# Performance work log

Hardware: AMD Instinct MI355X
Metric: run time of the kernel (lower is better)

Reference implementation:

```python
import jax, jax.numpy as jnp
import numpy as np

B, D, H, DH, NQ, NK = 64, 768, 8, 128, 256, 256


def _ln(x, g, b, eps=1e-5):
    m = x.mean(-1, keepdims=True)
    v = ((x - m) ** 2).mean(-1, keepdims=True)
    return (x - m) / jnp.sqrt(v + eps) * g + b


def setup_inputs() -> dict:
    key = jax.random.key(0)
    ks = jax.random.split(key, 16)
    w = lambda k, s: jax.random.normal(k, s, jnp.float32) * 0.02
    return {
        'emb_cause': jax.random.normal(ks[0], (B, D), jnp.float32),
        'emb_action': jax.random.normal(ks[1], (B, D), jnp.float32),
        'tok_cause': jax.random.normal(ks[2], (B, NK, D), jnp.float32),
        'tok_effect': jax.random.normal(ks[3], (B, NQ, D), jnp.float32),
        'fuse_ln_g': jnp.ones(2 * D), 'fuse_ln_b': jnp.zeros(2 * D),
        'fuse_w1': w(ks[4], (2 * D, D)), 'fuse_b1': jnp.zeros(D),
        'fuse_w2': w(ks[5], (D, D)), 'fuse_b2': jnp.zeros(D),
        'delta_ln_g': jnp.ones(D), 'delta_ln_b': jnp.zeros(D),
        'delta_w': w(ks[6], (D, D)), 'delta_b': jnp.zeros(D),
        'qg_w': w(ks[7], (D, H * DH)), 'qg_b': jnp.zeros(H * DH),
        'kg_w': w(ks[8], (D, H * DH)), 'kg_b': jnp.zeros(H * DH),
        'eff_ln_g': jnp.ones(D), 'eff_ln_b': jnp.zeros(D),
        'eff_w1': w(ks[9], (D, D)), 'eff_b1': jnp.zeros(D),
        'eff_w2': w(ks[10], (D, D)), 'eff_b2': jnp.zeros(D),
        'u_w': w(ks[11], (D, H * DH)),
        'v_w': w(ks[12], (D, H * DH)),
        'logit_scale': jnp.zeros(()),
    }


def reference(emb_cause, emb_action, tok_cause, tok_effect,
              fuse_ln_g, fuse_ln_b, fuse_w1, fuse_b1, fuse_w2, fuse_b2,
              delta_ln_g, delta_ln_b, delta_w, delta_b,
              qg_w, qg_b, kg_w, kg_b,
              eff_ln_g, eff_ln_b, eff_w1, eff_b1, eff_w2, eff_b2,
              u_w, v_w, logit_scale):
    # fuse: LN -> Linear -> GELU(exact) -> Linear (dropout = identity, eval)
    ctx_in = jnp.concatenate([emb_cause, emb_action], axis=-1)  # (B, 2D)
    h = jax.nn.gelu(_ln(ctx_in, fuse_ln_g, fuse_ln_b) @ fuse_w1 + fuse_b1, approximate=False)
    ctx = h @ fuse_w2 + fuse_b2  # (B, D)

    delta_e = _ln(ctx, delta_ln_g, delta_ln_b) @ delta_w + delta_b  # (B, D)
    pooled_effect = tok_effect.mean(axis=1)  # (B, D)
    e_shifted = pooled_effect + delta_e

    eh = jax.nn.gelu(_ln(ctx, eff_ln_g, eff_ln_b) @ eff_w1 + eff_b1, approximate=False)
    effect_pred = eh @ eff_w2 + eff_b2  # (B, D)

    q_gate = 1.0 + jnp.tanh(jax.nn.silu(ctx @ qg_w + qg_b)).reshape(B, H, DH)
    k_gate = 1.0 + jnp.tanh(jax.nn.silu(ctx @ kg_w + kg_b)).reshape(B, H, DH)

    # logit bias: torch code materializes (B,H,Nq,Nk,Dh); equivalent math is a
    # per-head inner product u.v (independent of q) broadcast over Nq.
    u = (e_shifted @ u_w).reshape(B, H, DH)            # (B, H, Dh)
    v = (tok_cause @ v_w).reshape(B, NK, H, DH)        # (B, Nk, H, Dh)
    bias = jnp.einsum('bhd,bkhd->bhk', u, v) / np.float32(np.sqrt(DH))
    logit_bias = jnp.exp(logit_scale) * jnp.broadcast_to(bias[:, :, None, :], (B, H, NQ, NK))

    return (q_gate, k_gate, e_shifted, delta_e, logit_bias, effect_pred)
```

## Files before the change

kernel.cpp:

```cpp
#include <hip/hip_runtime.h>
#include <math.h>

#define TPB 256

typedef float vf4 __attribute__((ext_vector_type(4)));

__global__ __launch_bounds__(256) void k_front(const float* __restrict__ ec, const float* __restrict__ ea,
                        const float* __restrict__ g, const float* __restrict__ bb,
                        float* __restrict__ o,
                        const float* __restrict__ tok_effect, float* __restrict__ pp)
{
    int t = threadIdx.x;
    if (blockIdx.x < 64) {
        int r = blockIdx.x;
        __shared__ float red[4];
        float v[6];
        float sum = 0.f;
#pragma unroll
        for (int j = 0; j < 6; ++j) {
            int c = t + j * TPB;
            float x = (c < 768) ? ec[r * 768 + c] : ea[r * 768 + (c - 768)];
            v[j] = x; sum += x;
        }
#pragma unroll
        for (int o_ = 32; o_ > 0; o_ >>= 1) sum += __shfl_xor(sum, o_);
        if ((t & 63) == 0) red[t >> 6] = sum;
        __syncthreads();
        sum = red[0] + red[1] + red[2] + red[3];
        float mean = sum * (1.0f / 1536.0f);
        __syncthreads();
        float s2 = 0.f;
#pragma unroll
        for (int j = 0; j < 6; ++j) { float d = v[j] - mean; s2 += d * d; }
#pragma unroll
        for (int o_ = 32; o_ > 0; o_ >>= 1) s2 += __shfl_xor(s2, o_);
        if ((t & 63) == 0) red[t >> 6] = s2;
        __syncthreads();
        s2 = red[0] + red[1] + red[2] + red[3];
        float rstd = rsqrtf(s2 * (1.0f / 1536.0f) + 1e-5f);
#pragma unroll
        for (int j = 0; j < 6; ++j) {
            int c = t + j * TPB;
            o[r * 1536 + c] = (v[j] - mean) * rstd * g[c] + bb[c];
        }
    } else {
        int m = blockIdx.x - 64;
        int cchunk = m % 3;
        int b = (m / 3) % 64;
        int qz = m / 192;
        int c = cchunk * TPB + t;
        const float* base = tok_effect + (size_t)(b * 256 + qz * 64) * 768 + c;
        float s = 0.f;
#pragma unroll 8
        for (int q = 0; q < 64; ++q) s += base[(size_t)q * 768];
        pp[(qz * 64 + b) * 768 + c] = s;
    }
}

struct GArgs {
    const float* X[4]; const float* W[4];
    int tile0[5];
    int nseg; int K; int kslice; int totN;
    float* part;
};

__global__ __launch_bounds__(256) void k_gemmp(GArgs A)
{
    const int ct = blockIdx.x, s = blockIdx.y;
    const int t = threadIdx.x;
    int seg = 0;
    while (seg + 1 < A.nseg && ct >= A.tile0[seg + 1]) ++seg;
    const float* __restrict__ X = A.X[seg];
    const float* __restrict__ W = A.W[seg];
    const int N = (A.tile0[seg + 1] - A.tile0[seg]) * 64;
    const int cb = (ct - A.tile0[seg]) * 64;
    const int tr4 = (t >> 4) << 2;
    const int tc4 = (t & 15) << 2;
    const int k0 = s * A.kslice;
    __shared__ float xs[32][64];
    __shared__ float wt[32][68];
    float acc[4][4] = {{0.f,0.f,0.f,0.f},{0.f,0.f,0.f,0.f},{0.f,0.f,0.f,0.f},{0.f,0.f,0.f,0.f}};
    for (int kc = 0; kc < A.kslice; kc += 32) {
        for (int n = t; n < 64 * 32; n += TPB) {
            int r = n >> 5, k = n & 31;
            xs[k][r] = X[r * A.K + k0 + kc + k];
        }
        for (int n = t; n < 32 * 64; n += TPB) {
            int k = n >> 6, c = n & 63;
            wt[k][c] = W[(size_t)(k0 + kc + k) * N + cb + c];
        }
        __syncthreads();
#pragma unroll
        for (int k = 0; k < 32; ++k) {
            float4 xv = *(const float4*)&xs[k][tr4];
            float4 wv = *(const float4*)&wt[k][tc4];
            acc[0][0] += xv.x * wv.x; acc[0][1] += xv.x * wv.y; acc[0][2] += xv.x * wv.z; acc[0][3] += xv.x * wv.w;
            acc[1][0] += xv.y * wv.x; acc[1][1] += xv.y * wv.y; acc[1][2] += xv.y * wv.z; acc[1][3] += xv.y * wv.w;
            acc[2][0] += xv.z * wv.x; acc[2][1] += xv.z * wv.y; acc[2][2] += xv.z * wv.z; acc[2][3] += xv.z * wv.w;
            acc[3][0] += xv.w * wv.x; acc[3][1] += xv.w * wv.y; acc[3][2] += xv.w * wv.z; acc[3][3] += xv.w * wv.w;
        }
        __syncthreads();
    }
    float* pp = A.part + (size_t)(s * 64 + tr4) * A.totN + ct * 64 + tc4;
#pragma unroll
    for (int i = 0; i < 4; ++i)
#pragma unroll
        for (int j = 0; j < 4; ++j)
            pp[i * A.totN + j] = acc[i][j];
}

struct EpiArgs {
    const float* part; const float* pp;
    const float* bias[4]; float* Y[4]; float* Y2[4];
    int col0[5]; int act[4]; int nseg; int totN; int S;
};

__global__ __launch_bounds__(256) void k_epi(EpiArgs A)
{
    int idx = blockIdx.x * TPB + threadIdx.x;
    if (idx >= 64 * A.totN) return;
    int r = idx / A.totN;
    int c = idx - r * A.totN;
    float v = 0.f;
    for (int s = 0; s < A.S; ++s) v += A.part[(size_t)(s * 64 + r) * A.totN + c];
    int seg = 0;
    while (seg + 1 < A.nseg && c >= A.col0[seg + 1]) ++seg;
    int cl = c - A.col0[seg];
    if (A.bias[seg]) v += A.bias[seg][cl];
    int act = A.act[seg];
    if (act == 1) {
        v = 0.5f * v * (1.0f + erff(v * 0.70710678118654752f));
    } else if (act == 2) {
        float si = v / (1.0f + expf(-v));
        v = 1.0f + tanhf(si);
    }
    int n = A.col0[seg + 1] - A.col0[seg];
    A.Y[seg][(size_t)r * n + cl] = v;
    if (A.Y2[seg]) {
        float s4 = A.pp[r * 768 + cl] + A.pp[(64 + r) * 768 + cl]
                 + A.pp[(128 + r) * 768 + cl] + A.pp[(192 + r) * 768 + cl];
        A.Y2[seg][(size_t)r * n + cl] = s4 * (1.0f / 256.0f) + v;
    }
}

__global__ __launch_bounds__(256) void k_epi_ln(const float* __restrict__ part, const float* __restrict__ b2,
                         const float* __restrict__ dg, const float* __restrict__ db,
                         const float* __restrict__ eg, const float* __restrict__ eb,
                         float* __restrict__ ctx, float* __restrict__ od, float* __restrict__ oe)
{
    int r = blockIdx.x, t = threadIdx.x;
    __shared__ float red[4];
    float v[3];
    float sum = 0.f;
#pragma unroll
    for (int j = 0; j < 3; ++j) {
        int c = t + j * TPB;
        float x = b2[c];
#pragma unroll
        for (int s = 0; s < 12; ++s) x += part[(s * 64 + r) * 768 + c];
        v[j] = x; sum += x;
        ctx[r * 768 + c] = x;
    }
#pragma unroll
    for (int o_ = 32; o_ > 0; o_ >>= 1) sum += __shfl_xor(sum, o_);
    if ((t & 63) == 0) red[t >> 6] = sum;
    __syncthreads();
    sum = red[0] + red[1] + red[2] + red[3];
    float mean = sum * (1.0f / 768.0f);
    __syncthreads();
    float s2 = 0.f;
#pragma unroll
    for (int j = 0; j < 3; ++j) { float d = v[j] - mean; s2 += d * d; }
#pragma unroll
    for (int o_ = 32; o_ > 0; o_ >>= 1) s2 += __shfl_xor(s2, o_);
    if ((t & 63) == 0) red[t >> 6] = s2;
    __syncthreads();
    s2 = red[0] + red[1] + red[2] + red[3];
    float rstd = rsqrtf(s2 * (1.0f / 768.0f) + 1e-5f);
#pragma unroll
    for (int j = 0; j < 3; ++j) {
        int c = t + j * TPB;
        float xh = (v[j] - mean) * rstd;
        od[r * 768 + c] = xh * dg[c] + db[c];
        oe[r * 768 + c] = xh * eg[c] + eb[c];
    }
}

__global__ __launch_bounds__(256) void k_wu(const float* __restrict__ u, const float* __restrict__ v_w,
                     float* __restrict__ wu)
{
    int h = blockIdx.x, ct = blockIdx.y;
    __shared__ float us[64][132];
    for (int n = threadIdx.x; n < 8192; n += TPB) {
        int b = n >> 7, d = n & 127;
        us[b][d] = u[b * 1024 + h * 128 + d];
    }
    __syncthreads();
    int c = ct * 64 + (threadIdx.x >> 2);
    int bo = threadIdx.x & 3;
    const float* vr = v_w + (size_t)c * 1024 + h * 128;
    float acc[16];
#pragma unroll
    for (int i = 0; i < 16; ++i) acc[i] = 0.f;
    for (int d = 0; d < 128; d += 4) {
        float4 w4 = *(const float4*)(vr + d);
#pragma unroll
        for (int i = 0; i < 16; ++i) {
            const float* ub = &us[4 * i + bo][d];
            acc[i] += w4.x * ub[0] + w4.y * ub[1] + w4.z * ub[2] + w4.w * ub[3];
        }
    }
#pragma unroll
    for (int i = 0; i < 16; ++i) {
        int b = 4 * i + bo;
        wu[(b * 8 + h) * 768 + c] = acc[i];
    }
}

__global__ __launch_bounds__(256) void k_bias2(const float* __restrict__ tok_cause, const float* __restrict__ wu,
                        const float* __restrict__ ls_ptr, float* __restrict__ bias_s)
{
    int b = blockIdx.x, kt = blockIdx.y;
    __shared__ float wuh[8][768];
    for (int n = threadIdx.x; n < 6144; n += TPB)
        ((float*)wuh)[n] = wu[b * 6144 + n];
    __syncthreads();
    const int lane = threadIdx.x & 63, w = threadIdx.x >> 6;
    float4 wur[3][8];
#pragma unroll
    for (int j = 0; j < 3; ++j)
#pragma unroll
        for (int h = 0; h < 8; ++h)
            wur[j][h] = *(const float4*)&wuh[h][(lane + 64 * j) * 4];
    float scale = expf(ls_ptr[0]) * 0.08838834764831845f;
#pragma unroll
    for (int rr = 0; rr < 4; ++rr) {
        int row = kt * 16 + w * 4 + rr;
        const float4* tr = (const float4*)(tok_cause + ((size_t)b * 256 + row) * 768);
        float4 t0 = tr[lane], t1 = tr[lane + 64], t2 = tr[lane + 128];
        float acc[8];
#pragma unroll
        for (int h = 0; h < 8; ++h) {
            acc[h] = t0.x * wur[0][h].x + t0.y * wur[0][h].y + t0.z * wur[0][h].z + t0.w * wur[0][h].w
                   + t1.x * wur[1][h].x + t1.y * wur[1][h].y + t1.z * wur[1][h].z + t1.w * wur[1][h].w
                   + t2.x * wur[2][h].x + t2.y * wur[2][h].y + t2.z * wur[2][h].z + t2.w * wur[2][h].w;
        }
#pragma unroll
        for (int h = 0; h < 8; ++h) {
            float vv = acc[h];
#pragma unroll
            for (int o_ = 32; o_ > 0; o_ >>= 1) vv += __shfl_xor(vv, o_);
            if (lane == 0) bias_s[(b * 8 + h) * 256 + row] = vv * scale;
        }
    }
}

__global__ __launch_bounds__(256) void k_broadcast(const float* __restrict__ bias_s, float* __restrict__ out)
{
    const vf4* b4 = (const vf4*)bias_s;
    vf4* o4 = (vf4*)out;
    unsigned i = blockIdx.x * TPB + threadIdx.x;
#pragma unroll
    for (int j = 0; j < 16; ++j) {
        unsigned idx = i + (unsigned)j * (2048u * TPB);
        vf4 v = b4[(idx >> 14) * 64 + (idx & 63)];
        __builtin_nontemporal_store(v, &o4[idx]);
    }
}

extern "C" void kernel_launch(void* const* d_in, const int* in_sizes, int n_in,
                              void* d_out, int out_size, void* d_ws, size_t ws_size,
                              hipStream_t stream)
{
    (void)in_sizes; (void)n_in; (void)out_size; (void)ws_size;
    const float* emb_cause  = (const float*)d_in[0];
    const float* emb_action = (const float*)d_in[1];
    const float* tok_cause  = (const float*)d_in[2];
    const float* tok_effect = (const float*)d_in[3];
    const float* fuse_ln_g  = (const float*)d_in[4];
    const float* fuse_ln_b  = (const float*)d_in[5];
    const float* fuse_w1    = (const float*)d_in[6];
    const float* fuse_b1    = (const float*)d_in[7];
    const float* fuse_w2    = (const float*)d_in[8];
    const float* fuse_b2    = (const float*)d_in[9];
    const float* delta_ln_g = (const float*)d_in[10];
    const float* delta_ln_b = (const float*)d_in[11];
    const float* delta_w    = (const float*)d_in[12];
    const float* delta_b    = (const float*)d_in[13];
    const float* qg_w       = (const float*)d_in[14];
    const float* qg_b       = (const float*)d_in[15];
    const float* kg_w       = (const float*)d_in[16];
    const float* kg_b       = (const float*)d_in[17];
    const float* eff_ln_g   = (const float*)d_in[18];
    const float* eff_ln_b   = (const float*)d_in[19];
    const float* eff_w1     = (const float*)d_in[20];
    const float* eff_b1     = (const float*)d_in[21];
    const float* eff_w2     = (const float*)d_in[22];
    const float* eff_b2     = (const float*)d_in[23];
    const float* u_w        = (const float*)d_in[24];
    const float* v_w        = (const float*)d_in[25];
    const float* logit_sc   = (const float*)d_in[26];

    float* ws = (float*)d_ws;
    float* cat_ln = ws + 0;
    float* h_buf  = ws + 98304;
    float* ctx    = ws + 147456;
    float* dln    = ws + 196608;
    float* eln    = ws + 245760;
    float* eh     = ws + 294912;
    float* u_buf  = ws + 344064;
    float* wu     = ws + 409600;
    float* pp     = ws + 802816;
    float* bias_s = ws + 999424;

    float* out    = (float*)d_out;
    float* out_qg = out + 0;
    float* out_kg = out + 65536;
    float* out_es = out + 131072;
    float* out_de = out + 180224;
    float* out_lb = out + 229376;
    float* out_ep = out + 33783808;

    float* part = out_lb + 20000000;

    k_front<<<832, TPB, 0, stream>>>(emb_cause, emb_action, fuse_ln_g, fuse_ln_b, cat_ln,
                                     tok_effect, pp);

    {
        GArgs A = {};
        A.X[0] = cat_ln; A.W[0] = fuse_w1;
        A.tile0[0] = 0; A.tile0[1] = 12;
        A.nseg = 1; A.K = 1536; A.kslice = 128; A.totN = 768; A.part = part;
        k_gemmp<<<dim3(12, 12), TPB, 0, stream>>>(A);
        EpiArgs E = {};
        E.part = part; E.pp = nullptr;
        E.bias[0] = fuse_b1; E.Y[0] = h_buf; E.Y2[0] = nullptr;
        E.col0[0] = 0; E.col0[1] = 768; E.act[0] = 1;
        E.nseg = 1; E.totN = 768; E.S = 12;
        k_epi<<<192, TPB, 0, stream>>>(E);
    }

    {
        GArgs A = {};
        A.X[0] = h_buf; A.W[0] = fuse_w2;
        A.tile0[0] = 0; A.tile0[1] = 12;
        A.nseg = 1; A.K = 768; A.kslice = 64; A.totN = 768; A.part = part;
        k_gemmp<<<dim3(12, 12), TPB, 0, stream>>>(A);
        k_epi_ln<<<64, TPB, 0, stream>>>(part, fuse_b2, delta_ln_g, delta_ln_b,
                                         eff_ln_g, eff_ln_b, ctx, dln, eln);
    }

    {
        GArgs A = {};
        A.X[0] = dln;  A.W[0] = delta_w;
        A.X[1] = eln;  A.W[1] = eff_w1;
        A.X[2] = ctx;  A.W[2] = qg_w;
        A.X[3] = ctx;  A.W[3] = kg_w;
        A.tile0[0] = 0; A.tile0[1] = 12; A.tile0[2] = 24; A.tile0[3] = 40; A.tile0[4] = 56;
        A.nseg = 4; A.K = 768; A.kslice = 64; A.totN = 3584; A.part = part;
        k_gemmp<<<dim3(56, 12), TPB, 0, stream>>>(A);
        EpiArgs E = {};
        E.part = part; E.pp = pp;
        E.bias[0] = delta_b; E.Y[0] = out_de; E.Y2[0] = out_es; E.act[0] = 0;
        E.bias[1] = eff_b1;  E.Y[1] = eh;     E.Y2[1] = nullptr; E.act[1] = 1;
        E.bias[2] = qg_b;    E.Y[2] = out_qg; E.Y2[2] = nullptr; E.act[2] = 2;
        E.bias[3] = kg_b;    E.Y[3] = out_kg; E.Y2[3] = nullptr; E.act[3] = 2;
        E.col0[0] = 0; E.col0[1] = 768; E.col0[2] = 1536; E.col0[3] = 2560; E.col0[4] = 3584;
        E.nseg = 4; E.totN = 3584; E.S = 12;
        k_epi<<<896, TPB, 0, stream>>>(E);
    }

    {
        GArgs A = {};
        A.X[0] = eh;     A.W[0] = eff_w2;
        A.X[1] = out_es; A.W[1] = u_w;
        A.tile0[0] = 0; A.tile0[1] = 12; A.tile0[2] = 28;
        A.nseg = 2; A.K = 768; A.kslice = 64; A.totN = 1792; A.part = part;
        k_gemmp<<<dim3(28, 12), TPB, 0, stream>>>(A);
        EpiArgs E = {};
        E.part = part; E.pp = nullptr;
        E.bias[0] = eff_b2;  E.Y[0] = out_ep; E.Y2[0] = nullptr; E.act[0] = 0;
        E.bias[1] = nullptr; E.Y[1] = u_buf;  E.Y2[1] = nullptr; E.act[1] = 0;
        E.col0[0] = 0; E.col0[1] = 768; E.col0[2] = 1792;
        E.nseg = 2; E.totN = 1792; E.S = 12;
        k_epi<<<448, TPB, 0, stream>>>(E);
    }

    k_wu<<<dim3(8, 12), TPB, 0, stream>>>(u_buf, v_w, wu);
    k_bias2<<<dim3(64, 16), TPB, 0, stream>>>(tok_cause, wu, logit_sc, bias_s);
    k_broadcast<<<2048, TPB, 0, stream>>>(bias_s, out_lb);
}
```

Before: 154.3 us.

## Fuse front-end GEMM chain into a single cooperative kernel with grid syncs

Replaces about ten separate launches (layernorm, pooling, split-K GEMMs, epilogues, wu) with one cooperative kernel of 256 blocks that uses grid.sync between stages. Split-K reductions plus bias and GELU are folded into the next GEMM's X-loader instead of running as separate epilogue kernels. Split-K factors also change (4 and 8 slices instead of 12). The aim is to cut launch overhead and intermediate round trips for these small GEMMs, at the cost of grid-sync latency, low occupancy (launch bounds of 1 block), and redundant reduction work inside the X loads.

```diff
diff --git a/kernel.cpp b/kernel.cpp
--- a/kernel.cpp
+++ b/kernel.cpp
@@ -1,99 +1,55 @@
 #include <hip/hip_runtime.h>
+#include <hip/hip_cooperative_groups.h>
 #include <math.h>
 
+namespace cg = cooperative_groups;
 #define TPB 256
 
 typedef float vf4 __attribute__((ext_vector_type(4)));
 
-__global__ __launch_bounds__(256) void k_front(const float* __restrict__ ec, const float* __restrict__ ea,
-                        const float* __restrict__ g, const float* __restrict__ bb,
-                        float* __restrict__ o,
-                        const float* __restrict__ tok_effect, float* __restrict__ pp)
-{
-    int t = threadIdx.x;
-    if (blockIdx.x < 64) {
-        int r = blockIdx.x;
-        __shared__ float red[4];
-        float v[6];
-        float sum = 0.f;
-#pragma unroll
-        for (int j = 0; j < 6; ++j) {
-            int c = t + j * TPB;
-            float x = (c < 768) ? ec[r * 768 + c] : ea[r * 768 + (c - 768)];
-            v[j] = x; sum += x;
-        }
-#pragma unroll
-        for (int o_ = 32; o_ > 0; o_ >>= 1) sum += __shfl_xor(sum, o_);
-        if ((t & 63) == 0) red[t >> 6] = sum;
-        __syncthreads();
-        sum = red[0] + red[1] + red[2] + red[3];
-        float mean = sum * (1.0f / 1536.0f);
-        __syncthreads();
-        float s2 = 0.f;
-#pragma unroll
-        for (int j = 0; j < 6; ++j) { float d = v[j] - mean; s2 += d * d; }
-#pragma unroll
-        for (int o_ = 32; o_ > 0; o_ >>= 1) s2 += __shfl_xor(s2, o_);
-        if ((t & 63) == 0) red[t >> 6] = s2;
-        __syncthreads();
-        s2 = red[0] + red[1] + red[2] + red[3];
-        float rstd = rsqrtf(s2 * (1.0f / 1536.0f) + 1e-5f);
-#pragma unroll
-        for (int j = 0; j < 6; ++j) {
-            int c = t + j * TPB;
-            o[r * 1536 + c] = (v[j] - mean) * rstd * g[c] + bb[c];
-        }
-    } else {
-        int m = blockIdx.x - 64;
-        int cchunk = m % 3;
-        int b = (m / 3) % 64;
-        int qz = m / 192;
-        int c = cchunk * TPB + t;
-        const float* base = tok_effect + (size_t)(b * 256 + qz * 64) * 768 + c;
-        float s = 0.f;
-#pragma unroll 8
-        for (int q = 0; q < 64; ++q) s += base[(size_t)q * 768];
-        pp[(qz * 64 + b) * 768 + c] = s;
-    }
-}
-
-struct GArgs {
-    const float* X[4]; const float* W[4];
-    int tile0[5];
-    int nseg; int K; int kslice; int totN;
-    float* part;
+__device__ __forceinline__ float gelu_f(float x) {
+    return 0.5f * x * (1.0f + erff(x * 0.70710678118654752f));
+}
+__device__ __forceinline__ float gate_f(float x) {
+    float si = x / (1.0f + expf(-x));
+    return 1.0f + tanhf(si);
+}
+
+struct CoopArgs {
+    const float *ec, *ea, *fln_g, *fln_b;
+    const float *tok_effect;
+    const float *fuse_w1, *fuse_b1, *fuse_w2, *fuse_b2;
+    const float *delta_ln_g, *delta_ln_b, *eff_ln_g, *eff_ln_b;
+    const float *delta_w, *delta_b, *eff_w1, *eff_b1, *eff_w2, *eff_b2;
+    const float *qg_w, *qg_b, *kg_w, *kg_b, *u_w, *v_w;
+    float *cat_ln, *ctx, *dln, *eln, *pp, *wu;
+    float *part1, *part2, *partA, *partB;
+    float *out_de, *out_es, *out_qg, *out_kg, *out_ep;
 };
 
-__global__ __launch_bounds__(256) void k_gemmp(GArgs A)
-{
-    const int ct = blockIdx.x, s = blockIdx.y;
+template <class XL>
+__device__ __forceinline__ void gemm_tile(XL xload, const float* __restrict__ W, int Wld, int cb,
+                                          int k0, int kslice, float* part, int totN, int gcol, int s,
+                                          float* xs, float* wt)
+{
     const int t = threadIdx.x;
-    int seg = 0;
-    while (seg + 1 < A.nseg && ct >= A.tile0[seg + 1]) ++seg;
-    const float* __restrict__ X = A.X[seg];
-    const float* __restrict__ W = A.W[seg];
-    const int N = (A.tile0[seg + 1] - A.tile0[seg]) * 64;
-    const int cb = (ct - A.tile0[seg]) * 64;
     const int tr4 = (t >> 4) << 2;
     const int tc4 = (t & 15) << 2;
-    const int k0 = s * A.kslice;
-    __shared__ float xs[32][64];
-    __shared__ float wt[32][68];
     float acc[4][4] = {{0.f,0.f,0.f,0.f},{0.f,0.f,0.f,0.f},{0.f,0.f,0.f,0.f},{0.f,0.f,0.f,0.f}};
-    for (int kc = 0; kc < A.kslice; kc += 32) {
-        for (int n = t; n < 64 * 32; n += TPB) {
+    for (int kc = 0; kc < kslice; kc += 32) {
+        for (int n = t; n < 2048; n += TPB) {
             int r = n >> 5, k = n & 31;
-            xs[k][r] = X[r * A.K + k0 + kc + k];
-        }
-        for (int n = t; n < 32 * 64; n += TPB) {
+            xs[(k << 6) + r] = xload(r, k0 + kc + k);
+        }
+        for (int n = t; n < 2048; n += TPB) {
             int k = n >> 6, c = n & 63;
-            wt[k][c] = W[(size_t)(k0 + kc + k) * N + cb + c];
+            wt[k * 68 + c] = W[(size_t)(k0 + kc + k) * Wld + cb + c];
         }
         __syncthreads();
 #pragma unroll
         for (int k = 0; k < 32; ++k) {
-            float4 xv = *(const float4*)&xs[k][tr4];
-            float4 wv = *(const float4*)&wt[k][tc4];
+            float4 xv = *(const float4*)&xs[(k << 6) + tr4];
+            float4 wv = *(const float4*)&wt[k * 68 + tc4];
             acc[0][0] += xv.x * wv.x; acc[0][1] += xv.x * wv.y; acc[0][2] += xv.x * wv.z; acc[0][3] += xv.x * wv.w;
             acc[1][0] += xv.y * wv.x; acc[1][1] += xv.y * wv.y; acc[1][2] += xv.y * wv.z; acc[1][3] += xv.y * wv.w;
             acc[2][0] += xv.z * wv.x; acc[2][1] += xv.z * wv.y; acc[2][2] += xv.z * wv.z; acc[2][3] += xv.z * wv.w;
@@ -101,119 +57,225 @@
         }
         __syncthreads();
     }
-    float* pp = A.part + (size_t)(s * 64 + tr4) * A.totN + ct * 64 + tc4;
+    float* pp = part + (size_t)(s * 64 + tr4) * totN + gcol + tc4;
 #pragma unroll
     for (int i = 0; i < 4; ++i)
 #pragma unroll
         for (int j = 0; j < 4; ++j)
-            pp[i * A.totN + j] = acc[i][j];
-}
-
-struct EpiArgs {
-    const float* part; const float* pp;
-    const float* bias[4]; float* Y[4]; float* Y2[4];
-    int col0[5]; int act[4]; int nseg; int totN; int S;
-};
-
-__global__ __launch_bounds__(256) void k_epi(EpiArgs A)
-{
-    int idx = blockIdx.x * TPB + threadIdx.x;
-    if (idx >= 64 * A.totN) return;
-    int r = idx / A.totN;
-    int c = idx - r * A.totN;
-    float v = 0.f;
-    for (int s = 0; s < A.S; ++s) v += A.part[(size_t)(s * 64 + r) * A.totN + c];
-    int seg = 0;
-    while (seg + 1 < A.nseg && c >= A.col0[seg + 1]) ++seg;
-    int cl = c - A.col0[seg];
-    if (A.bias[seg]) v += A.bias[seg][cl];
-    int act = A.act[seg];
-    if (act == 1) {
-        v = 0.5f * v * (1.0f + erff(v * 0.70710678118654752f));
-    } else if (act == 2) {
-        float si = v / (1.0f + expf(-v));
-        v = 1.0f + tanhf(si);
-    }
-    int n = A.col0[seg + 1] - A.col0[seg];
-    A.Y[seg][(size_t)r * n + cl] = v;
-    if (A.Y2[seg]) {
-        float s4 = A.pp[r * 768 + cl] + A.pp[(64 + r) * 768 + cl]
-                 + A.pp[(128 + r) * 768 + cl] + A.pp[(192 + r) * 768 + cl];
-        A.Y2[seg][(size_t)r * n + cl] = s4 * (1.0f / 256.0f) + v;
-    }
-}
-
-__global__ __launch_bounds__(256) void k_epi_ln(const float* __restrict__ part, const float* __restrict__ b2,
-                         const float* __restrict__ dg, const float* __restrict__ db,
-                         const float* __restrict__ eg, const float* __restrict__ eb,
-                         float* __restrict__ ctx, float* __restrict__ od, float* __restrict__ oe)
-{
-    int r = blockIdx.x, t = threadIdx.x;
+            pp[i * totN + j] = acc[i][j];
+}
+
+__global__ __launch_bounds__(TPB, 1) void k_coop(CoopArgs A)
+{
+    __shared__ float smem[8448];
     __shared__ float red[4];
-    float v[3];
-    float sum = 0.f;
-#pragma unroll
-    for (int j = 0; j < 3; ++j) {
-        int c = t + j * TPB;
-        float x = b2[c];
-#pragma unroll
-        for (int s = 0; s < 12; ++s) x += part[(s * 64 + r) * 768 + c];
-        v[j] = x; sum += x;
-        ctx[r * 768 + c] = x;
-    }
-#pragma unroll
-    for (int o_ = 32; o_ > 0; o_ >>= 1) sum += __shfl_xor(sum, o_);
-    if ((t & 63) == 0) red[t >> 6] = sum;
-    __syncthreads();
-    sum = red[0] + red[1] + red[2] + red[3];
-    float mean = sum * (1.0f / 768.0f);
-    __syncthreads();
-    float s2 = 0.f;
-#pragma unroll
-    for (int j = 0; j < 3; ++j) { float d = v[j] - mean; s2 += d * d; }
-#pragma unroll
-    for (int o_ = 32; o_ > 0; o_ >>= 1) s2 += __shfl_xor(s2, o_);
-    if ((t & 63) == 0) red[t >> 6] = s2;
-    __syncthreads();
-    s2 = red[0] + red[1] + red[2] + red[3];
-    float rstd = rsqrtf(s2 * (1.0f / 768.0f) + 1e-5f);
-#pragma unroll
-    for (int j = 0; j < 3; ++j) {
-        int c = t + j * TPB;
-        float xh = (v[j] - mean) * rstd;
-        od[r * 768 + c] = xh * dg[c] + db[c];
-        oe[r * 768 + c] = xh * eg[c] + eb[c];
-    }
-}
-
-__global__ __launch_bounds__(256) void k_wu(const float* __restrict__ u, const float* __restrict__ v_w,
-                     float* __restrict__ wu)
-{
-    int h = blockIdx.x, ct = blockIdx.y;
-    __shared__ float us[64][132];
-    for (int n = threadIdx.x; n < 8192; n += TPB) {
-        int b = n >> 7, d = n & 127;
-        us[b][d] = u[b * 1024 + h * 128 + d];
-    }
-    __syncthreads();
-    int c = ct * 64 + (threadIdx.x >> 2);
-    int bo = threadIdx.x & 3;
-    const float* vr = v_w + (size_t)c * 1024 + h * 128;
-    float acc[16];
-#pragma unroll
-    for (int i = 0; i < 16; ++i) acc[i] = 0.f;
-    for (int d = 0; d < 128; d += 4) {
-        float4 w4 = *(const float4*)(vr + d);
+    float* xs = smem;
+    float* wt = smem + 2048;
+    cg::grid_group grid = cg::this_grid();
+    const int blk = blockIdx.x, t = threadIdx.x;
+
+    if (blk < 64) {
+        int r = blk;
+        float v[6]; float sum = 0.f;
+#pragma unroll
+        for (int j = 0; j < 6; ++j) {
+            int c = t + j * TPB;
+            float x = (c < 768) ? A.ec[r * 768 + c] : A.ea[r * 768 + (c - 768)];
+            v[j] = x; sum += x;
+        }
+#pragma unroll
+        for (int o_ = 32; o_ > 0; o_ >>= 1) sum += __shfl_xor(sum, o_);
+        if ((t & 63) == 0) red[t >> 6] = sum;
+        __syncthreads();
+        sum = red[0] + red[1] + red[2] + red[3];
+        float mean = sum * (1.f / 1536.f);
+        __syncthreads();
+        float s2 = 0.f;
+#pragma unroll
+        for (int j = 0; j < 6; ++j) { float d = v[j] - mean; s2 += d * d; }
+#pragma unroll
+        for (int o_ = 32; o_ > 0; o_ >>= 1) s2 += __shfl_xor(s2, o_);
+        if ((t & 63) == 0) red[t >> 6] = s2;
+        __syncthreads();
+        s2 = red[0] + red[1] + red[2] + red[3];
+        float rstd = rsqrtf(s2 * (1.f / 1536.f) + 1e-5f);
+#pragma unroll
+        for (int j = 0; j < 6; ++j) {
+            int c = t + j * TPB;
+            A.cat_ln[r * 1536 + c] = (v[j] - mean) * rstd * A.fln_g[c] + A.fln_b[c];
+        }
+    }
+#pragma unroll
+    for (int i = 0; i < 3; ++i) {
+        int m = blk * 3 + i;
+        int cch = m % 3, b = (m / 3) % 64, qz = m / 192;
+        int c = cch * TPB + t;
+        const float* base = A.tok_effect + (size_t)(b * 256 + qz * 64) * 768 + c;
+        float s = 0.f;
+#pragma unroll 16
+        for (int q = 0; q < 64; ++q) s += base[(size_t)q * 768];
+        A.pp[(qz * 64 + b) * 768 + c] = s;
+    }
+    grid.sync();
+
+    if (blk < 144) {
+        int ct = blk % 12, s = blk / 12;
+        const float* cl = A.cat_ln;
+        auto xl = [&](int r, int k) { return cl[r * 1536 + k]; };
+        gemm_tile(xl, A.fuse_w1, 768, ct * 64, s * 128, 128, A.part1, 768, ct * 64, s, xs, wt);
+    }
+    grid.sync();
+
+    if (blk < 144) {
+        int ct = blk % 12, s = blk / 12;
+        const float* p1 = A.part1; const float* b1 = A.fuse_b1;
+        auto xl = [&](int r, int k) {
+            float v = b1[k];
+#pragma unroll
+            for (int q = 0; q < 12; ++q) v += p1[(size_t)(q * 64 + r) * 768 + k];
+            return gelu_f(v);
+        };
+        gemm_tile(xl, A.fuse_w2, 768, ct * 64, s * 64, 64, A.part2, 768, ct * 64, s, xs, wt);
+    }
+    grid.sync();
+
+    if (blk < 64) {
+        int r = blk;
+        float v[3]; float sum = 0.f;
+#pragma unroll
+        for (int j = 0; j < 3; ++j) {
+            int c = t + j * TPB;
+            float x = A.fuse_b2[c];
+#pragma unroll
+            for (int s = 0; s < 12; ++s) x += A.part2[(size_t)(s * 64 + r) * 768 + c];
+            v[j] = x; sum += x;
+            A.ctx[r * 768 + c] = x;
+        }
+#pragma unroll
+        for (int o_ = 32; o_ > 0; o_ >>= 1) sum += __shfl_xor(sum, o_);
+        if ((t & 63) == 0) red[t >> 6] = sum;
+        __syncthreads();
+        sum = red[0] + red[1] + red[2] + red[3];
+        float mean = sum * (1.f / 768.f);
+        __syncthreads();
+        float s2 = 0.f;
+#pragma unroll
+        for (int j = 0; j < 3; ++j) { float d = v[j] - mean; s2 += d * d; }
+#pragma unroll
+        for (int o_ = 32; o_ > 0; o_ >>= 1) s2 += __shfl_xor(s2, o_);
+        if ((t & 63) == 0) red[t >> 6] = s2;
+        __syncthreads();
+        s2 = red[0] + red[1] + red[2] + red[3];
+        float rstd = rsqrtf(s2 * (1.f / 768.f) + 1e-5f);
+#pragma unroll
+        for (int j = 0; j < 3; ++j) {
+            int c = t + j * TPB;
+            float xh = (v[j] - mean) * rstd;
+            A.dln[r * 768 + c] = xh * A.delta_ln_g[c] + A.delta_ln_b[c];
+            A.eln[r * 768 + c] = xh * A.eff_ln_g[c] + A.eff_ln_b[c];
+        }
+    }
+    grid.sync();
+
+    if (blk < 224) {
+        int ct = blk % 56, s = blk / 56;
+        const float* X; const float* W; int Wld, cb;
+        if (ct < 12)      { X = A.dln; W = A.delta_w; Wld = 768;  cb = ct * 64; }
+        else if (ct < 24) { X = A.eln; W = A.eff_w1;  Wld = 768;  cb = (ct - 12) * 64; }
+        else if (ct < 40) { X = A.ctx; W = A.qg_w;    Wld = 1024; cb = (ct - 24) * 64; }
+        else              { X = A.ctx; W = A.kg_w;    Wld = 1024; cb = (ct - 40) * 64; }
+        auto xl = [&](int r, int k) { return X[r * 768 + k]; };
+        gemm_tile(xl, W, Wld, cb, s * 192, 192, A.partA, 3584, ct * 64, s, xs, wt);
+    }
+    grid.sync();
+
+    if (blk < 32) {
+#pragma unroll
+        for (int ii = 0; ii < 28; ++ii) {
+            int idx = blk * TPB + t + ii * 8192;
+            int r = idx / 3584, c = idx - r * 3584;
+            if (c >= 768 && c < 1536) continue;
+            float v = A.partA[(size_t)r * 3584 + c] + A.partA[(size_t)(64 + r) * 3584 + c]
+                    + A.partA[(size_t)(128 + r) * 3584 + c] + A.partA[(size_t)(192 + r) * 3584 + c];
+            if (c < 768) {
+                float de = v + A.delta_b[c];
+                A.out_de[r * 768 + c] = de;
+                float s4 = A.pp[r * 768 + c] + A.pp[(64 + r) * 768 + c]
+                         + A.pp[(128 + r) * 768 + c] + A.pp[(192 + r) * 768 + c];
+                A.out_es[r * 768 + c] = de + s4 * (1.f / 256.f);
+            } else if (c < 2560) {
+                A.out_qg[r * 1024 + (c - 1536)] = gate_f(v + A.qg_b[c - 1536]);
+            } else {
+                A.out_kg[r * 1024 + (c - 2560)] = gate_f(v + A.kg_b[c - 2560]);
+            }
+        }
+    } else {
+        int m = blk - 32;
+        int ct = m % 28, s = m / 28;
+        if (ct < 12) {
+            const float* pA = A.partA; const float* b1 = A.eff_b1;
+            auto xl = [&](int r, int k) {
+                float v = b1[k];
+#pragma unroll
+                for (int q = 0; q < 4; ++q) v += pA[(size_t)(q * 64 + r) * 3584 + 768 + k];
+                return gelu_f(v);
+            };
+            gemm_tile(xl, A.eff_w2, 768, ct * 64, s * 96, 96, A.partB, 1792, ct * 64, s, xs, wt);
+        } else {
+            const float* pA = A.partA; const float* ppp = A.pp; const float* db = A.delta_b;
+            auto xl = [&](int r, int k) {
+                float v = db[k];
+#pragma unroll
+                for (int q = 0; q < 4; ++q) v += pA[(size_t)(q * 64 + r) * 3584 + k];
+                float s4 = ppp[r * 768 + k] + ppp[(64 + r) * 768 + k]
+                         + ppp[(128 + r) * 768 + k] + ppp[(192 + r) * 768 + k];
+                return v + s4 * (1.f / 256.f);
+            };
+            gemm_tile(xl, A.u_w, 1024, (ct - 12) * 64, s * 96, 96, A.partB, 1792, ct * 64, s, xs, wt);
+        }
+    }
+    grid.sync();
+
+    if (blk < 32) {
+#pragma unroll
+        for (int ii = 0; ii < 6; ++ii) {
+            int idx = blk * TPB + t + ii * 8192;
+            int r = idx / 768, c = idx - r * 768;
+            float v = A.eff_b2[c];
+#pragma unroll
+            for (int q = 0; q < 8; ++q) v += A.partB[(size_t)(q * 64 + r) * 1792 + c];
+            A.out_ep[r * 768 + c] = v;
+        }
+    } else if (blk < 128) {
+        int m = blk - 32;
+        int h = m / 12, ctile = m % 12;
+        for (int n = t; n < 8192; n += TPB) {
+            int b = n >> 7, d = n & 127;
+            float v = 0.f;
+#pragma unroll
+            for (int q = 0; q < 8; ++q) v += A.partB[(size_t)(q * 64 + b) * 1792 + 768 + h * 128 + d];
+            smem[b * 132 + d] = v;
+        }
+        __syncthreads();
+        int c = ctile * 64 + (t >> 2);
+        int bo = t & 3;
+        const float* vr = A.v_w + (size_t)c * 1024 + h * 128;
+        float acc[16];
+#pragma unroll
+        for (int i = 0; i < 16; ++i) acc[i] = 0.f;
+        for (int d = 0; d < 128; d += 4) {
+            float4 w4 = *(const float4*)(vr + d);
+#pragma unroll
+            for (int i = 0; i < 16; ++i) {
+                const float* ub = &smem[(4 * i + bo) * 132 + d];
+                acc[i] += w4.x * ub[0] + w4.y * ub[1] + w4.z * ub[2] + w4.w * ub[3];
+            }
+        }
 #pragma unroll
         for (int i = 0; i < 16; ++i) {
-            const float* ub = &us[4 * i + bo][d];
-            acc[i] += w4.x * ub[0] + w4.y * ub[1] + w4.z * ub[2] + w4.w * ub[3];
-        }
-    }
-#pragma unroll
-    for (int i = 0; i < 16; ++i) {
-        int b = 4 * i + bo;
-        wu[(b * 8 + h) * 768 + c] = acc[i];
+            int b = 4 * i + bo;
+            A.wu[(b * 8 + h) * 768 + c] = acc[i];
+        }
     }
 }
 
@@ -273,45 +335,17 @@
                               hipStream_t stream)
 {
     (void)in_sizes; (void)n_in; (void)out_size; (void)ws_size;
-    const float* emb_cause  = (const float*)d_in[0];
-    const float* emb_action = (const float*)d_in[1];
     const float* tok_cause  = (const float*)d_in[2];
-    const float* tok_effect = (const float*)d_in[3];
-    const float* fuse_ln_g  = (const float*)d_in[4];
-    const float* fuse_ln_b  = (const float*)d_in[5];
-    const float* fuse_w1    = (const float*)d_in[6];
-    const float* fuse_b1    = (const float*)d_in[7];
-    const float* fuse_w2    = (const float*)d_in[8];
-    const float* fuse_b2    = (const float*)d_in[9];
-    const float* delta_ln_g = (const float*)d_in[10];
-    const float* delta_ln_b = (const float*)d_in[11];
-    const float* delta_w    = (const float*)d_in[12];
-    const float* delta_b    = (const float*)d_in[13];
-    const float* qg_w       = (const float*)d_in[14];
-    const float* qg_b       = (const float*)d_in[15];
-    const float* kg_w       = (const float*)d_in[16];
-    const float* kg_b       = (const float*)d_in[17];
-    const float* eff_ln_g   = (const float*)d_in[18];
-    const float* eff_ln_b   = (const float*)d_in[19];
-    const float* eff_w1     = (const float*)d_in[20];
-    const float* eff_b1     = (const float*)d_in[21];
-    const float* eff_w2     = (const float*)d_in[22];
-    const float* eff_b2     = (const float*)d_in[23];
-    const float* u_w        = (const float*)d_in[24];
-    const float* v_w        = (const float*)d_in[25];
     const float* logit_sc   = (const float*)d_in[26];
 
     float* ws = (float*)d_ws;
     float* cat_ln = ws + 0;
-    float* h_buf  = ws + 98304;
-    float* ctx    = ws + 147456;
-    float* dln    = ws + 196608;
-    float* eln    = ws + 245760;
-    float* eh     = ws + 294912;
-    float* u_buf  = ws + 344064;
-    float* wu     = ws + 409600;
-    float* pp     = ws + 802816;
-    float* bias_s = ws + 999424;
+    float* ctx    = ws + 98304;
+    float* dln    = ws + 147456;
+    float* eln    = ws + 196608;
+    float* pp     = ws + 245760;
+    float* wu     = ws + 442368;
+    float* bias_s = ws + 835584;
 
     float* out    = (float*)d_out;
     float* out_qg = out + 0;
@@ -321,72 +355,33 @@
     float* out_lb = out + 229376;
     float* out_ep = out + 33783808;
 
-    float* part = out_lb + 20000000;
-
-    k_front<<<832, TPB, 0, stream>>>(emb_cause, emb_action, fuse_ln_g, fuse_ln_b, cat_ln,
-                                     tok_effect, pp);
-
-    {
-        GArgs A = {};
-        A.X[0] = cat_ln; A.W[0] = fuse_w1;
-        A.tile0[0] = 0; A.tile0[1] = 12;
-        A.nseg = 1; A.K = 1536; A.kslice = 128; A.totN = 768; A.part = part;
-        k_gemmp<<<dim3(12, 12), TPB, 0, stream>>>(A);
-        EpiArgs E = {};
-        E.part = part; E.pp = nullptr;
-        E.bias[0] = fuse_b1; E.Y[0] = h_buf; E.Y2[0] = nullptr;
-        E.col0[0] = 0; E.col0[1] = 768; E.act[0] = 1;
-        E.nseg = 1; E.totN = 768; E.S = 12;
-        k_epi<<<192, TPB, 0, stream>>>(E);
-    }
-
-    {
-        GArgs A = {};
-        A.X[0] = h_buf; A.W[0] = fuse_w2;
-        A.tile0[0] = 0; A.tile0[1] = 12;
-        A.nseg = 1; A.K = 768; A.kslice = 64; A.totN = 768; A.part = part;
-        k_gemmp<<<dim3(12, 12), TPB, 0, stream>>>(A);
-        k_epi_ln<<<64, TPB, 0, stream>>>(part, fuse_b2, delta_ln_g, delta_ln_b,
-                                         eff_ln_g, eff_ln_b, ctx, dln, eln);
-    }
-
-    {
-        GArgs A = {};
-        A.X[0] = dln;  A.W[0] = delta_w;
-        A.X[1] = eln;  A.W[1] = eff_w1;
-        A.X[2] = ctx;  A.W[2] = qg_w;
-        A.X[3] = ctx;  A.W[3] = kg_w;
-        A.tile0[0] = 0; A.tile0[1] = 12; A.tile0[2] = 24; A.tile0[3] = 40; A.tile0[4] = 56;
-        A.nseg = 4; A.K = 768; A.kslice = 64; A.totN = 3584; A.part = part;
-        k_gemmp<<<dim3(56, 12), TPB, 0, stream>>>(A);
-        EpiArgs E = {};
-        E.part = part; E.pp = pp;
-        E.bias[0] = delta_b; E.Y[0] = out_de; E.Y2[0] = out_es; E.act[0] = 0;
-        E.bias[1] = eff_b1;  E.Y[1] = eh;     E.Y2[1] = nullptr; E.act[1] = 1;
-        E.bias[2] = qg_b;    E.Y[2] = out_qg; E.Y2[2] = nullptr; E.act[2] = 2;
-        E.bias[3] = kg_b;    E.Y[3] = out_kg; E.Y2[3] = nullptr; E.act[3] = 2;
-        E.col0[0] = 0; E.col0[1] = 768; E.col0[2] = 1536; E.col0[3] = 2560; E.col0[4] = 3584;
-        E.nseg = 4; E.totN = 3584; E.S = 12;
-        k_epi<<<896, TPB, 0, stream>>>(E);
-    }
-
-    {
-        GArgs A = {};
-        A.X[0] = eh;     A.W[0] = eff_w2;
-        A.X[1] = out_es; A.W[1] = u_w;
-        A.tile0[0] = 0; A.tile0[1] = 12; A.tile0[2] = 28;
-        A.nseg = 2; A.K = 768; A.kslice = 64; A.totN = 1792; A.part = part;
-        k_gemmp<<<dim3(28, 12), TPB, 0, stream>>>(A);
-        EpiArgs E = {};
-        E.part = part; E.pp = nullptr;
-        E.bias[0] = eff_b2;  E.Y[0] = out_ep; E.Y2[0] = nullptr; E.act[0] = 0;
-        E.bias[1] = nullptr; E.Y[1] = u_buf;  E.Y2[1] = nullptr; E.act[1] = 0;
-        E.col0[0] = 0; E.col0[1] = 768; E.col0[2] = 1792;
-        E.nseg = 2; E.totN = 1792; E.S = 12;
-        k_epi<<<448, TPB, 0, stream>>>(E);
-    }
-
-    k_wu<<<dim3(8, 12), TPB, 0, stream>>>(u_buf, v_w, wu);
+    float* pbase = out_lb + 20000000;
+    float* part1 = pbase;
+    float* part2 = pbase + 589824;
+    float* partA = pbase + 1179648;
+    float* partB = pbase + 2097152;
+
+    CoopArgs A;
+    A.ec = (const float*)d_in[0];  A.ea = (const float*)d_in[1];
+    A.fln_g = (const float*)d_in[4]; A.fln_b = (const float*)d_in[5];
+    A.tok_effect = (const float*)d_in[3];
+    A.fuse_w1 = (const float*)d_in[6];  A.fuse_b1 = (const float*)d_in[7];
+    A.fuse_w2 = (const float*)d_in[8];  A.fuse_b2 = (const float*)d_in[9];
+    A.delta_ln_g = (const float*)d_in[10]; A.delta_ln_b = (const float*)d_in[11];
+    A.eff_ln_g = (const float*)d_in[18];   A.eff_ln_b = (const float*)d_in[19];
+    A.delta_w = (const float*)d_in[12]; A.delta_b = (const float*)d_in[13];
+    A.eff_w1 = (const float*)d_in[20];  A.eff_b1 = (const float*)d_in[21];
+    A.eff_w2 = (const float*)d_in[22];  A.eff_b2 = (const float*)d_in[23];
+    A.qg_w = (const float*)d_in[14]; A.qg_b = (const float*)d_in[15];
+    A.kg_w = (const float*)d_in[16]; A.kg_b = (const float*)d_in[17];
+    A.u_w = (const float*)d_in[24];  A.v_w = (const float*)d_in[25];
+    A.cat_ln = cat_ln; A.ctx = ctx; A.dln = dln; A.eln = eln; A.pp = pp; A.wu = wu;
+    A.part1 = part1; A.part2 = part2; A.partA = partA; A.partB = partB;
+    A.out_de = out_de; A.out_es = out_es; A.out_qg = out_qg; A.out_kg = out_kg; A.out_ep = out_ep;
+
+    void* kargs[] = { (void*)&A };
+    hipLaunchCooperativeKernel((const void*)k_coop, dim3(256), dim3(TPB), kargs, 0, stream);
+
     k_bias2<<<dim3(64, 16), TPB, 0, stream>>>(tok_cause, wu, logit_sc, bias_s);
     k_broadcast<<<2048, TPB, 0, stream>>>(bias_s, out_lb);
 }
```

After: 355.2 us. 2.3x slower.
